# Performance work log

Measured on AMD Instinct MI355X. Metric: run time of the kernel, lower is better.

The kernel has to match this reference:

```python
import jax, jax.numpy as jnp
import numpy as np

B, S, HID = 1, 4096, 2048
H, HKV, D = 16, 4, 128
BLOCK = 32          # dllm_block_length
EPS = 1e-6
SCALE = D ** -0.5


def setup_inputs() -> dict:
    key = jax.random.key(0)
    ks = jax.random.split(key, 4)
    hidden_states = jax.random.normal(ks[0], (B, S, HID), dtype=jnp.float32)
    # RoPE tables (interleaved-half convention), shape [S, D]
    inv_freq = 1.0 / (10000.0 ** (np.arange(0, D, 2, dtype=np.float32) / D))
    t = np.arange(S, dtype=np.float32)
    freqs = np.outer(t, inv_freq)                      # [S, D/2]
    emb = np.concatenate([freqs, freqs], axis=-1)      # [S, D]
    cos = jnp.asarray(np.cos(emb), dtype=jnp.float32)
    sin = jnp.asarray(np.sin(emb), dtype=jnp.float32)
    w_qkv = jax.random.normal(ks[1], (HID, (H + 2 * HKV) * D), dtype=jnp.float32) * (HID ** -0.5)
    w_o = jax.random.normal(ks[2], (H * D, HID), dtype=jnp.float32) * ((H * D) ** -0.5)
    q_norm_w = jnp.ones((D,), dtype=jnp.float32)
    k_norm_w = jnp.ones((D,), dtype=jnp.float32)
    return {"hidden_states": hidden_states, "cos": cos, "sin": sin,
            "w_qkv": w_qkv, "q_norm_w": q_norm_w, "k_norm_w": k_norm_w, "w_o": w_o}


def _rms_norm(x, w):
    var = jnp.mean(jnp.square(x), axis=-1, keepdims=True)
    return x * jax.lax.rsqrt(var + EPS) * w


def _rotate_half(x):
    x1, x2 = jnp.split(x, 2, axis=-1)
    return jnp.concatenate([-x2, x1], axis=-1)


def reference(hidden_states, cos, sin, w_qkv, q_norm_w, k_norm_w, w_o):
    b, s, _ = hidden_states.shape
    qkv = hidden_states @ w_qkv                                   # [B,S,(H+2Hkv)*D]
    q = qkv[..., : H * D].reshape(b, s, H, D)
    k = qkv[..., H * D: (H + HKV) * D].reshape(b, s, HKV, D)
    v = qkv[..., (H + HKV) * D:].reshape(b, s, HKV, D)
    # per-head RMSNorm on q/k (use_qk_norm)
    q = _rms_norm(q, q_norm_w)
    k = _rms_norm(k, k_norm_w)
    # RoPE
    c = cos[None, :, None, :]
    sn = sin[None, :, None, :]
    q = q * c + _rotate_half(q) * sn
    k = k * c + _rotate_half(k) * sn
    # GQA: repeat kv heads
    rep = H // HKV
    k = jnp.repeat(k, rep, axis=2)                                # [B,S,H,D]
    v = jnp.repeat(v, rep, axis=2)
    scores = jnp.einsum("bshd,bthd->bhst", q, k) * SCALE          # [B,H,S,S]
    # block-diffusion mask: bidirectional within a dllm block, causal across blocks
    blk = jnp.arange(s) // BLOCK
    allowed = blk[None, :] <= blk[:, None]                        # [S,S]
    scores = jnp.where(allowed[None, None], scores, jnp.finfo(scores.dtype).min)
    attn = jax.nn.softmax(scores, axis=-1)
    out = jnp.einsum("bhst,bthd->bshd", attn, v).reshape(b, s, H * D)
    return out @ w_o
```

## Files before the change

### kernel.cpp

```cpp
#include <hip/hip_runtime.h>
#include <cstdint>

typedef __bf16 bf16;
typedef __attribute__((ext_vector_type(4))) __bf16 bf16x4;
typedef __attribute__((ext_vector_type(8))) __bf16 bf16x8;
typedef __attribute__((ext_vector_type(4))) float f32x4;

#define MFMA16(a, b, c) __builtin_amdgcn_mfma_f32_16x16x32_bf16((a), (b), (c), 0, 0, 0)

static __device__ __forceinline__ void gload16(const void* g, void* l) {
  __builtin_amdgcn_global_load_lds(
      (const __attribute__((address_space(1))) void*)g,
      (__attribute__((address_space(3))) void*)l, 16, 0, 0);
}

#define SWZ128(r, k) ((r) * 128 + ((k) ^ (((r) & 7) << 3)))
#define SWZP(r, k)   ((r) * 64  + ((k) ^ (((r) & 7) << 3)))
#define SWZV(r, k)   ((r) * 64  + ((k) ^ (((r) & 7) << 3)))

__global__ __launch_bounds__(256) void k_convert(const float* __restrict__ in,
                                                 bf16* __restrict__ out, int n4) {
  int i = blockIdx.x * blockDim.x + threadIdx.x;
  if (i >= n4) return;
  float4 v = *(const float4*)&in[(size_t)i * 4];
  bf16x4 o;
  o[0] = (bf16)v.x; o[1] = (bf16)v.y; o[2] = (bf16)v.z; o[3] = (bf16)v.w;
  *(bf16x4*)&out[(size_t)i * 4] = o;
}

__global__ void k_transpose(const float* __restrict__ in, bf16* __restrict__ out,
                            int R, int C) {
  __shared__ float tile[32][33];
  int bx = blockIdx.x, by = blockIdx.y;
  int tx = threadIdx.x, ty = threadIdx.y;
#pragma unroll
  for (int i = ty; i < 32; i += 8)
    tile[i][tx] = in[(size_t)(by * 32 + i) * C + bx * 32 + tx];
  __syncthreads();
#pragma unroll
  for (int i = ty; i < 32; i += 8)
    out[(size_t)(bx * 32 + i) * R + by * 32 + tx] = (bf16)tile[tx][i];
}

__global__ void k_vtrans(const bf16* __restrict__ qkv, bf16* __restrict__ vtg) {
  __shared__ bf16 tile[32][33];
  int s0 = blockIdx.x * 32, d0 = blockIdx.y * 32, hk = blockIdx.z;
  int tx = threadIdx.x, ty = threadIdx.y;
#pragma unroll
  for (int i = ty; i < 32; i += 8)
    tile[i][tx] = qkv[(size_t)(s0 + i) * 3072 + 2560 + hk * 128 + d0 + tx];
  __syncthreads();
#pragma unroll
  for (int i = ty; i < 32; i += 8)
    vtg[(size_t)hk * 524288 + (size_t)(d0 + i) * 4096 + s0 + tx] = tile[tx][i];
}

template <typename OutT>
__global__ __launch_bounds__(256) void k_gemm(const bf16* __restrict__ A,
                                              const bf16* __restrict__ BT,
                                              OutT* __restrict__ C, int M, int N, int K) {
  __shared__ bf16 As[128 * 32];
  __shared__ bf16 Bs[128 * 32];
  const int tid = threadIdx.x;
  const int wv = tid >> 6, lane = tid & 63;
  const int lr = lane & 15, lg = lane >> 4;
  const int wm = (wv >> 1) * 64, wn = (wv & 1) * 64;
  const int bm = blockIdx.x, bn = blockIdx.y;
  const size_t baseA = (size_t)bm * 128 * K;
  const size_t baseB = (size_t)bn * 128 * K;
  f32x4 acc[4][4] = {};
  for (int kt = 0; kt < K; kt += 32) {
    __syncthreads();
#pragma unroll
    for (int inst = 0; inst < 2; ++inst) {
      int ch = inst * 256 + tid;
      int row = ch >> 2, ko = (ch & 3) * 8;
      gload16(A + baseA + (size_t)row * K + kt + ko, &As[(size_t)(inst * 256 + wv * 64) * 8]);
      gload16(BT + baseB + (size_t)row * K + kt + ko, &Bs[(size_t)(inst * 256 + wv * 64) * 8]);
    }
    __syncthreads();
    bf16x8 af[4], bfr[4];
#pragma unroll
    for (int mi = 0; mi < 4; ++mi) af[mi] = *(const bf16x8*)&As[(wm + mi * 16 + lr) * 32 + lg * 8];
#pragma unroll
    for (int nj = 0; nj < 4; ++nj) bfr[nj] = *(const bf16x8*)&Bs[(wn + nj * 16 + lr) * 32 + lg * 8];
#pragma unroll
    for (int mi = 0; mi < 4; ++mi)
#pragma unroll
      for (int nj = 0; nj < 4; ++nj)
        acc[mi][nj] = MFMA16(af[mi], bfr[nj], acc[mi][nj]);
  }
#pragma unroll
  for (int mi = 0; mi < 4; ++mi)
#pragma unroll
    for (int nj = 0; nj < 4; ++nj)
#pragma unroll
      for (int j = 0; j < 4; ++j) {
        int r = bm * 128 + wm + mi * 16 + lg * 4 + j;
        int c = bn * 128 + wn + nj * 16 + lr;
        C[(size_t)r * N + c] = (OutT)acc[mi][nj][j];
      }
}

__global__ __launch_bounds__(256) void k_rmsrope(bf16* __restrict__ qkv,
                                                 const float* __restrict__ cosb,
                                                 const float* __restrict__ sinb,
                                                 const float* __restrict__ qw,
                                                 const float* __restrict__ kw) {
  int row = blockIdx.x * 4 + (threadIdx.x >> 6);
  int lane = threadIdx.x & 63;
  int s = row / 20, hd = row % 20;
  bool isq = hd < 16;
  int col = isq ? hd * 128 : 2048 + (hd - 16) * 128;
  bf16* p = qkv + (size_t)s * 3072 + col;
  float x1 = (float)p[lane], x2 = (float)p[lane + 64];
  float ss = x1 * x1 + x2 * x2;
#pragma unroll
  for (int m = 32; m; m >>= 1) ss += __shfl_xor(ss, m);
  float r = rsqrtf(ss * (1.0f / 128.0f) + 1e-6f);
  const float* w = isq ? qw : kw;
  float y1 = x1 * r * w[lane], y2 = x2 * r * w[lane + 64];
  float c1 = cosb[s * 128 + lane], c2 = cosb[s * 128 + lane + 64];
  float s1 = sinb[s * 128 + lane], s2 = sinb[s * 128 + lane + 64];
  p[lane] = (bf16)(y1 * c1 - y2 * s1);
  p[lane + 64] = (bf16)(y2 * c2 + y1 * s2);
}

__global__ __launch_bounds__(512, 2) void k_attn(const bf16* __restrict__ qkv,
                                                 const bf16* __restrict__ vtg,
                                                 bf16* __restrict__ out) {
  __shared__ bf16 Ks[64 * 128];
  __shared__ bf16 Pl[128 * 64];
  __shared__ bf16 Vt[128 * 64];
  const int tid = threadIdx.x;
  const int wv = tid >> 6, lane = tid & 63;
  const int lr = lane & 15, lg = lane >> 4;
  const int u = blockIdx.x & 255, vsl = blockIdx.x >> 8;
  const int h = u & 15;
  const int qa = u >> 4;
  const int qt = vsl ? (31 - qa) : qa;
  const int q0 = qt * 128;
  const int hk = h >> 2;
  const int wq = wv * 16;
  const float K2 = 0.12751744f;

  bf16x8 qf[4];
  {
    const bf16* qrow = qkv + (size_t)(q0 + wq + lr) * 3072 + h * 128 + lg * 8;
#pragma unroll
    for (int kk = 0; kk < 4; ++kk) qf[kk] = *(const bf16x8*)(qrow + kk * 32);
  }

  f32x4 oacc[8] = {};
  float mst[4], lst[4];
#pragma unroll
  for (int j = 0; j < 4; ++j) { mst[j] = -1e30f; lst[j] = 0.f; }

  const int nkb = 2 * qt + 2;
  for (int kb = 0; kb < nkb; ++kb) {
    const int t0 = kb * 64;
    __syncthreads();
#pragma unroll
    for (int inst = 0; inst < 2; ++inst) {
      int ch = inst * 512 + tid;
      int row = ch >> 4;
      int doff = ((ch & 15) * 8) ^ ((row & 7) << 3);
      gload16(qkv + (size_t)(t0 + row) * 3072 + 2048 + hk * 128 + doff,
              &Ks[(size_t)(inst * 512 + wv * 64) * 8]);
    }
#pragma unroll
    for (int inst = 0; inst < 2; ++inst) {
      int ch = inst * 512 + tid;
      int drow = ch >> 3;
      int koff = ((ch & 7) * 8) ^ ((drow & 7) << 3);
      gload16(vtg + (size_t)hk * 524288 + (size_t)drow * 4096 + t0 + koff,
              &Vt[(size_t)(inst * 512 + wv * 64) * 8]);
    }
    __syncthreads();

    f32x4 sacc[4] = {};
#pragma unroll
    for (int kk = 0; kk < 4; ++kk) {
      bf16x8 bk[4];
#pragma unroll
      for (int nj = 0; nj < 4; ++nj)
        bk[nj] = *(const bf16x8*)&Ks[SWZ128(nj * 16 + lr, kk * 32 + lg * 8)];
#pragma unroll
      for (int nj = 0; nj < 4; ++nj)
        sacc[nj] = MFMA16(qf[kk], bk[nj], sacc[nj]);
    }

    const bool maskt = (kb >= 2 * qt);
    const int koff2 = (kb - 2 * qt) * 64;
    float rowm[4];
#pragma unroll
    for (int j = 0; j < 4; ++j) rowm[j] = -1e30f;
#pragma unroll
    for (int nj = 0; nj < 4; ++nj)
#pragma unroll
      for (int j = 0; j < 4; ++j) {
        float sv = sacc[nj][j] * K2;
        if (maskt && (koff2 + nj * 16 + lr > ((wq + lg * 4 + j) | 31))) sv = -1e30f;
        sacc[nj][j] = sv;
        rowm[j] = fmaxf(rowm[j], sv);
      }
#pragma unroll
    for (int j = 0; j < 4; ++j)
#pragma unroll
      for (int mm = 1; mm < 16; mm <<= 1)
        rowm[j] = fmaxf(rowm[j], __shfl_xor(rowm[j], mm));
    bool need = false;
#pragma unroll
    for (int j = 0; j < 4; ++j) need |= (rowm[j] - mst[j] > 8.0f);
    if (__any(need)) {
#pragma unroll
      for (int j = 0; j < 4; ++j) {
        float mnew = fmaxf(mst[j], rowm[j]);
        float al = exp2f(mst[j] - mnew);
        mst[j] = mnew;
        lst[j] *= al;
#pragma unroll
        for (int dj = 0; dj < 8; ++dj) oacc[dj][j] *= al;
      }
    }
    float rs[4] = {0.f, 0.f, 0.f, 0.f};
#pragma unroll
    for (int nj = 0; nj < 4; ++nj)
#pragma unroll
      for (int j = 0; j < 4; ++j) {
        float p = exp2f(sacc[nj][j] - mst[j]);
        rs[j] += p;
        Pl[SWZP(wq + lg * 4 + j, nj * 16 + lr)] = (bf16)p;
      }
#pragma unroll
    for (int j = 0; j < 4; ++j) {
#pragma unroll
      for (int mm = 1; mm < 16; mm <<= 1) rs[j] += __shfl_xor(rs[j], mm);
      lst[j] += rs[j];
    }

#pragma unroll
    for (int kk = 0; kk < 2; ++kk) {
      bf16x8 ap = *(const bf16x8*)&Pl[SWZP(wq + lr, kk * 32 + lg * 8)];
#pragma unroll
      for (int dj = 0; dj < 8; ++dj) {
        bf16x8 bv = *(const bf16x8*)&Vt[SWZV(dj * 16 + lr, kk * 32 + lg * 8)];
        oacc[dj] = MFMA16(ap, bv, oacc[dj]);
      }
    }
  }

#pragma unroll
  for (int j = 0; j < 4; ++j) lst[j] = 1.0f / lst[j];
#pragma unroll
  for (int dj = 0; dj < 8; ++dj)
#pragma unroll
    for (int j = 0; j < 4; ++j) {
      int srow = q0 + wq + lg * 4 + j;
      int d = dj * 16 + lr;
      out[(size_t)srow * 2048 + h * 128 + d] = (bf16)(oacc[dj][j] * lst[j]);
    }
}

extern "C" void kernel_launch(void* const* d_in, const int* in_sizes, int n_in,
                              void* d_out, int out_size, void* d_ws, size_t ws_size,
                              hipStream_t stream) {
  const float* hs = (const float*)d_in[0];
  const float* cosb = (const float*)d_in[1];
  const float* sinb = (const float*)d_in[2];
  const float* w_qkv = (const float*)d_in[3];
  const float* qw = (const float*)d_in[4];
  const float* kw = (const float*)d_in[5];
  const float* w_o = (const float*)d_in[6];
  float* out = (float*)d_out;

  char* ws = (char*)d_ws;
  bf16* qkv   = (bf16*)(ws);
  bf16* hsb   = (bf16*)(ws + 25165824);
  bf16* wqkvT = (bf16*)(ws + 41943040);
  bf16* woT   = (bf16*)(ws + 41943040);
  bf16* attno = (bf16*)(ws + 25165824);
  bf16* vtg   = (bf16*)(ws + 54525952);

  k_convert<<<8192, 256, 0, stream>>>(hs, hsb, 2097152);
  k_transpose<<<dim3(96, 64), dim3(32, 8), 0, stream>>>(w_qkv, wqkvT, 2048, 3072);
  k_gemm<bf16><<<dim3(32, 24), 256, 0, stream>>>(hsb, wqkvT, qkv, 4096, 3072, 2048);
  k_rmsrope<<<20480, 256, 0, stream>>>(qkv, cosb, sinb, qw, kw);
  k_vtrans<<<dim3(128, 4, 4), dim3(32, 8), 0, stream>>>(qkv, vtg);
  k_transpose<<<dim3(64, 64), dim3(32, 8), 0, stream>>>(w_o, woT, 2048, 2048);
  k_attn<<<512, 512, 0, stream>>>(qkv, vtg, attno);
  k_gemm<float><<<dim3(32, 16), 256, 0, stream>>>(attno, woT, out, 4096, 2048, 2048);
}
```

Before: 332.7 us.

## Prefetch next K/V tile into registers and raise attention occupancy hint

Replaces the direct global-to-LDS loads of K and V^T with register prefetch. Each iteration stores the already-loaded registers into shared memory, then issues global loads for the next tile so they overlap the current tile's QK and PV compute. The launch bound's minimum-blocks hint also rises from 2 to 4, which caps per-thread registers and may cause spills alongside the extra prefetch registers.

Measured after the change: 415.6 us. +24.9%, slower.

```diff
diff --git a/kernel.cpp b/kernel.cpp
--- a/kernel.cpp
+++ b/kernel.cpp
@@ -126,7 +126,7 @@
   p[lane + 64] = (bf16)(y2 * c2 + y1 * s2);
 }
 
-__global__ __launch_bounds__(512, 2) void k_attn(const bf16* __restrict__ qkv,
+__global__ __launch_bounds__(512, 4) void k_attn(const bf16* __restrict__ qkv,
                                                  const bf16* __restrict__ vtg,
                                                  bf16* __restrict__ out) {
   __shared__ bf16 Ks[64 * 128];
@@ -144,6 +144,13 @@
   const int wq = wv * 16;
   const float K2 = 0.12751744f;
 
+  const int rowK0 = tid >> 4;
+  const int doffK = ((tid & 15) * 8) ^ ((rowK0 & 7) << 3);
+  const int drow0 = tid >> 3;
+  const int koffV = ((tid & 7) * 8) ^ ((drow0 & 7) << 3);
+  const bf16* kbase = qkv + 2048 + hk * 128 + doffK;
+  const bf16* vbase = vtg + (size_t)hk * 524288 + koffV;
+
   bf16x8 qf[4];
   {
     const bf16* qrow = qkv + (size_t)(q0 + wq + lr) * 3072 + h * 128 + lg * 8;
@@ -157,26 +164,26 @@
   for (int j = 0; j < 4; ++j) { mst[j] = -1e30f; lst[j] = 0.f; }
 
   const int nkb = 2 * qt + 2;
+
+  bf16x8 kr0 = *(const bf16x8*)(kbase + (size_t)rowK0 * 3072);
+  bf16x8 kr1 = *(const bf16x8*)(kbase + (size_t)(rowK0 + 32) * 3072);
+  bf16x8 vr0 = *(const bf16x8*)(vbase + (size_t)drow0 * 4096);
+  bf16x8 vr1 = *(const bf16x8*)(vbase + (size_t)(drow0 + 64) * 4096);
+
   for (int kb = 0; kb < nkb; ++kb) {
-    const int t0 = kb * 64;
     __syncthreads();
-#pragma unroll
-    for (int inst = 0; inst < 2; ++inst) {
-      int ch = inst * 512 + tid;
-      int row = ch >> 4;
-      int doff = ((ch & 15) * 8) ^ ((row & 7) << 3);
-      gload16(qkv + (size_t)(t0 + row) * 3072 + 2048 + hk * 128 + doff,
-              &Ks[(size_t)(inst * 512 + wv * 64) * 8]);
-    }
-#pragma unroll
-    for (int inst = 0; inst < 2; ++inst) {
-      int ch = inst * 512 + tid;
-      int drow = ch >> 3;
-      int koff = ((ch & 7) * 8) ^ ((drow & 7) << 3);
-      gload16(vtg + (size_t)hk * 524288 + (size_t)drow * 4096 + t0 + koff,
-              &Vt[(size_t)(inst * 512 + wv * 64) * 8]);
-    }
+    *(bf16x8*)&Ks[(size_t)tid * 8] = kr0;
+    *(bf16x8*)&Ks[(size_t)(512 + tid) * 8] = kr1;
+    *(bf16x8*)&Vt[(size_t)tid * 8] = vr0;
+    *(bf16x8*)&Vt[(size_t)(512 + tid) * 8] = vr1;
     __syncthreads();
+    if (kb + 1 < nkb) {
+      const int t1 = (kb + 1) * 64;
+      kr0 = *(const bf16x8*)(kbase + (size_t)(t1 + rowK0) * 3072);
+      kr1 = *(const bf16x8*)(kbase + (size_t)(t1 + rowK0 + 32) * 3072);
+      vr0 = *(const bf16x8*)(vbase + (size_t)drow0 * 4096 + t1);
+      vr1 = *(const bf16x8*)(vbase + (size_t)(drow0 + 64) * 4096 + t1);
+    }
 
     f32x4 sacc[4] = {};
 #pragma unroll
```

## Double-buffer K tiles and overlap K/V loads with attention compute

Applied to the files above, without the earlier changes.

K tiles move into a two-slot LDS buffer, and the next tile is prefetched at the start of each iteration. The V tile load is issued before the QK^T and softmax work and is only waited on before the PV MFMAs, so global-to-LDS traffic overlaps compute instead of stalling at the top of the loop. The sync points move to before and after the PV stage. Per-thread load offsets are hoisted out of the loop. The cost is an extra 16KB of LDS per block, which could limit occupancy, and more complex synchronisation.

Result: no change. 331.2 us (-0.5%).

```diff
diff --git a/kernel.cpp b/kernel.cpp
--- a/kernel.cpp
+++ b/kernel.cpp
@@ -129,7 +129,7 @@
 __global__ __launch_bounds__(512, 2) void k_attn(const bf16* __restrict__ qkv,
                                                  const bf16* __restrict__ vtg,
                                                  bf16* __restrict__ out) {
-  __shared__ bf16 Ks[64 * 128];
+  __shared__ bf16 Ks[2][64 * 128];
   __shared__ bf16 Pl[128 * 64];
   __shared__ bf16 Vt[128 * 64];
   const int tid = threadIdx.x;
@@ -144,6 +144,18 @@
   const int wq = wv * 16;
   const float K2 = 0.12751744f;
 
+  const int chK0 = tid, chK1 = 512 + tid;
+  const int rowK0 = chK0 >> 4, rowK1 = chK1 >> 4;
+  const int doffK0 = ((chK0 & 15) * 8) ^ ((rowK0 & 7) << 3);
+  const int doffK1 = ((chK1 & 15) * 8) ^ ((rowK1 & 7) << 3);
+  const int drow0 = chK0 >> 3, drow1 = chK1 >> 3;
+  const int koffV0 = ((chK0 & 7) * 8) ^ ((drow0 & 7) << 3);
+  const int koffV1 = ((chK1 & 7) * 8) ^ ((drow1 & 7) << 3);
+  const bf16* kb0 = qkv + 2048 + hk * 128 + doffK0;
+  const bf16* kb1 = qkv + 2048 + hk * 128 + doffK1;
+  const bf16* vb0 = vtg + (size_t)hk * 524288 + (size_t)drow0 * 4096 + koffV0;
+  const bf16* vb1 = vtg + (size_t)hk * 524288 + (size_t)drow1 * 4096 + koffV1;
+
   bf16x8 qf[4];
   {
     const bf16* qrow = qkv + (size_t)(q0 + wq + lr) * 3072 + h * 128 + lg * 8;
@@ -157,26 +169,21 @@
   for (int j = 0; j < 4; ++j) { mst[j] = -1e30f; lst[j] = 0.f; }
 
   const int nkb = 2 * qt + 2;
+
+  gload16(kb0 + (size_t)rowK0 * 3072, &Ks[0][(size_t)(wv * 64) * 8]);
+  gload16(kb1 + (size_t)rowK1 * 3072, &Ks[0][(size_t)(512 + wv * 64) * 8]);
+  __syncthreads();
+
   for (int kb = 0; kb < nkb; ++kb) {
+    const int cur = kb & 1;
     const int t0 = kb * 64;
-    __syncthreads();
-#pragma unroll
-    for (int inst = 0; inst < 2; ++inst) {
-      int ch = inst * 512 + tid;
-      int row = ch >> 4;
-      int doff = ((ch & 15) * 8) ^ ((row & 7) << 3);
-      gload16(qkv + (size_t)(t0 + row) * 3072 + 2048 + hk * 128 + doff,
-              &Ks[(size_t)(inst * 512 + wv * 64) * 8]);
-    }
-#pragma unroll
-    for (int inst = 0; inst < 2; ++inst) {
-      int ch = inst * 512 + tid;
-      int drow = ch >> 3;
-      int koff = ((ch & 7) * 8) ^ ((drow & 7) << 3);
-      gload16(vtg + (size_t)hk * 524288 + (size_t)drow * 4096 + t0 + koff,
-              &Vt[(size_t)(inst * 512 + wv * 64) * 8]);
-    }
-    __syncthreads();
+    if (kb + 1 < nkb) {
+      const size_t t1 = (size_t)(kb + 1) * 64;
+      gload16(kb0 + (t1 + rowK0) * 3072, &Ks[cur ^ 1][(size_t)(wv * 64) * 8]);
+      gload16(kb1 + (t1 + rowK1) * 3072, &Ks[cur ^ 1][(size_t)(512 + wv * 64) * 8]);
+    }
+    gload16(vb0 + t0, &Vt[(size_t)(wv * 64) * 8]);
+    gload16(vb1 + t0, &Vt[(size_t)(512 + wv * 64) * 8]);
 
     f32x4 sacc[4] = {};
 #pragma unroll
@@ -184,7 +191,7 @@
       bf16x8 bk[4];
 #pragma unroll
       for (int nj = 0; nj < 4; ++nj)
-        bk[nj] = *(const bf16x8*)&Ks[SWZ128(nj * 16 + lr, kk * 32 + lg * 8)];
+        bk[nj] = *(const bf16x8*)&Ks[cur][SWZ128(nj * 16 + lr, kk * 32 + lg * 8)];
 #pragma unroll
       for (int nj = 0; nj < 4; ++nj)
         sacc[nj] = MFMA16(qf[kk], bk[nj], sacc[nj]);
@@ -239,6 +246,8 @@
       lst[j] += rs[j];
     }
 
+    __syncthreads();
+
 #pragma unroll
     for (int kk = 0; kk < 2; ++kk) {
       bf16x8 ap = *(const bf16x8*)&Pl[SWZP(wq + lr, kk * 32 + lg * 8)];
@@ -248,6 +257,7 @@
         oacc[dj] = MFMA16(ap, bv, oacc[dj]);
       }
     }
+    __syncthreads();
   }
 
 #pragma unroll
```
